# Kernel optimization log

Measured on AMD Instinct MI355X. Metric: run time of the kernel, lower is better.

## Reference

```python
import jax, jax.numpy as jnp
import numpy as np

N, D, H, F = 384, 512, 8, 64  # n_nodes, in/out features, heads, per-head hidden
SLOPE = 0.2


def gat_v2_layer(x, mask, W_l, W_r, a):
    """GATv2 layer (is_concat=True). x: [N, D_in]; mask: [N, N, 1] bool.

    torch semantics: g_sum[i, j] = g_l[j] + g_r[i]; e = a . LeakyReLU(g_sum);
    softmax over j (dim=1); aggregate g_r with einsum('ijh,jhf->ihf').
    attn linear nn.Linear(F, 1) is shared across heads -> a: [F].
    """
    n = x.shape[0]
    g_l = (x @ W_l).reshape(n, H, F)
    g_r = (x @ W_r).reshape(n, H, F)
    # pairwise [i, j, h, f] = g_r[i] + g_l[j]  (the big O(N^2) intermediate)
    s = jax.nn.leaky_relu(g_r[:, None] + g_l[None, :], negative_slope=SLOPE)
    e = jnp.einsum('ijhf,f->ijh', s, a)
    e = jnp.where(mask, e, -jnp.inf)
    att = jax.nn.softmax(e, axis=1)  # normalize over source nodes j
    out = jnp.einsum('ijh,jhf->ihf', att, g_r)
    return out.reshape(n, H * F)


def setup_inputs() -> dict:
    key = jax.random.key(0)
    ks = jax.random.split(key, 8)
    x = jax.random.normal(ks[0], (N, D), dtype=jnp.float32)
    adj = jax.random.randint(ks[1], (N, N, 1), 0, 2, dtype=jnp.int32)
    sd = 1.0 / np.sqrt(D)
    sa = 1.0 / np.sqrt(F)
    W_l0 = jax.random.normal(ks[2], (D, H * F), dtype=jnp.float32) * sd
    W_r0 = jax.random.normal(ks[3], (D, H * F), dtype=jnp.float32) * sd
    a0 = jax.random.normal(ks[4], (F,), dtype=jnp.float32) * sa
    W_l1 = jax.random.normal(ks[5], (H * F, H * F), dtype=jnp.float32) * sd
    W_r1 = jax.random.normal(ks[6], (H * F, H * F), dtype=jnp.float32) * sd
    a1 = jax.random.normal(ks[7], (F,), dtype=jnp.float32) * sa
    return {"x": x, "adj": adj, "W_l0": W_l0, "W_r0": W_r0, "a0": a0,
            "W_l1": W_l1, "W_r1": W_r1, "a1": a1}


def reference(x, adj, W_l0, W_r0, a0, W_l1, W_r1, a1):
    n = x.shape[0]
    # selfloop: fill diagonal of adj with 1
    idx = jnp.arange(n)
    adj = adj.at[idx, idx, 0].set(1)
    mask = adj != 0  # [N, N, 1]
    # layer 0: GATv2 -> ELU (i < n_layers-1) -> residual
    out = jax.nn.elu(gat_v2_layer(x, mask, W_l0, W_r0, a0))
    x = x + out
    # layer 1: GATv2 -> Identity -> residual
    out = gat_v2_layer(x, mask, W_l1, W_r1, a1)
    x = x + out
    return x
```

## Files before the change

kernel.cpp:

```cpp
#include <hip/hip_runtime.h>
#include <hip/hip_bf16.h>
#include <stdint.h>

typedef unsigned short ushort_t;
typedef unsigned long long u64;
typedef __attribute__((ext_vector_type(8))) short short8;
typedef __attribute__((ext_vector_type(4))) float f32x4;

#define N_NODES 384
#define HF      512
#define IT      12

__device__ inline ushort_t f2bf(float f) {
  __hip_bfloat16 b = __float2bfloat16(f);
  return *reinterpret_cast<ushort_t*>(&b);
}
__device__ inline float bf2f_u(ushort_t u) {
  union { float f; uint32_t i; } v; v.i = ((uint32_t)u) << 16; return v.f;
}
__device__ inline short8 pack8(const float* s) {
  short8 r;
#pragma unroll
  for (int j = 0; j < 8; ++j) r[j] = (short)f2bf(s[j]);
  return r;
}

__global__ __launch_bounds__(256) void gemm_direct(
    const float* __restrict__ X, const float* __restrict__ WL,
    const float* __restrict__ WR, float* __restrict__ G,
    ushort_t* __restrict__ glb, ushort_t* __restrict__ grT,
    const int* __restrict__ adj, u64* __restrict__ mbits)
{
  const int t = threadIdx.x, wave = t >> 6, lane = t & 63;
  const int lm = lane & 15, q = lane >> 4;
  const int m0 = blockIdx.x * 16;
  const int n0 = (blockIdx.y * 4 + wave) * 32;
  const float* Wp = (n0 < 512) ? (WL + n0) : (WR + (n0 - 512));
  const float* Arow = X + (m0 + lm) * HF;

  f32x4 acc0 = {0.f, 0.f, 0.f, 0.f};
  f32x4 acc1 = {0.f, 0.f, 0.f, 0.f};
#pragma unroll 4
  for (int kc = 0; kc < 16; ++kc) {
    const int kbase = kc * 32 + q * 8;
    float4 a0 = *(const float4*)(Arow + kbase);
    float4 a1 = *(const float4*)(Arow + kbase + 4);
    float av8[8] = {a0.x, a0.y, a0.z, a0.w, a1.x, a1.y, a1.z, a1.w};
    short8 af = pack8(av8);
    float b0f[8], b1f[8];
#pragma unroll
    for (int j = 0; j < 8; ++j) {
      const float* r = Wp + (kbase + j) * HF;
      b0f[j] = r[lm];
      b1f[j] = r[16 + lm];
    }
    short8 b0 = pack8(b0f);
    short8 b1 = pack8(b1f);
    acc0 = __builtin_amdgcn_mfma_f32_16x16x32_bf16(af, b0, acc0, 0, 0, 0);
    acc1 = __builtin_amdgcn_mfma_f32_16x16x32_bf16(af, b1, acc1, 0, 0, 0);
  }
  if (n0 < 512) {
#pragma unroll
    for (int r = 0; r < 4; ++r) {
      int m = m0 + q * 4 + r;
      glb[m * HF + n0 + lm]      = f2bf(acc0[r]);
      glb[m * HF + n0 + 16 + lm] = f2bf(acc1[r]);
    }
  } else {
#pragma unroll
    for (int r = 0; r < 4; ++r) {
      int m = m0 + q * 4 + r;
      G[m * 1024 + n0 + lm]      = acc0[r];
      G[m * 1024 + n0 + 16 + lm] = acc1[r];
    }
    int c0 = n0 - 512;
    uint2 p0, p1;
    p0.x = (uint32_t)f2bf(acc0[0]) | ((uint32_t)f2bf(acc0[1]) << 16);
    p0.y = (uint32_t)f2bf(acc0[2]) | ((uint32_t)f2bf(acc0[3]) << 16);
    p1.x = (uint32_t)f2bf(acc1[0]) | ((uint32_t)f2bf(acc1[1]) << 16);
    p1.y = (uint32_t)f2bf(acc1[2]) | ((uint32_t)f2bf(acc1[3]) << 16);
    *(uint2*)&grT[(c0 + lm) * 384 + m0 + q * 4]      = p0;
    *(uint2*)&grT[(c0 + 16 + lm) * 384 + m0 + q * 4] = p1;
  }
  if (adj != nullptr && blockIdx.y == 0) {
    int rbase = (blockIdx.x * 4 + wave) * 4;
    for (int rr = 0; rr < 4; ++rr) {
      int row = rbase + rr;
#pragma unroll
      for (int w = 0; w < 6; ++w) {
        int j = w * 64 + lane;
        u64 m = __ballot(adj[row * N_NODES + j] != 0 || row == j);
        if (lane == 0) mbits[row * 6 + w] = m;
      }
    }
  }
}

template <int LAYER>
__global__ __launch_bounds__(384) void attn_fused(
    const float* __restrict__ G, const ushort_t* __restrict__ glb,
    const ushort_t* __restrict__ grT, const u64* __restrict__ mbits,
    const float* __restrict__ resid_in, const float* __restrict__ avec,
    float* __restrict__ xcur_out, float* __restrict__ f_out)
{
  __shared__ __align__(16) char smem[55296];
  ushort_t (*s_gl)[72]     = (ushort_t(*)[72])smem;
  float    (*s_e)[N_NODES] = (float(*)[N_NODES])smem;
  ushort_t (*s_pb)[392]    = (ushort_t(*)[392])(smem + 18432);
  __shared__ float s_bri[IT];
  __shared__ u64   s_mask[IT][6];

  const int t = threadIdx.x;
  const int i0 = blockIdx.x * IT, h = blockIdx.y;
  const int lane = t & 63, wave = t >> 6;

  if (t < 72) ((u64*)s_mask)[t] = mbits[i0 * 6 + t];
  if (t >= 128 && t < 320) {
    int u = t - 128, il = u >> 4, fg = u & 15;
    float4 g4 = *(const float4*)(G + (i0 + il) * 1024 + 512 + h * 64 + fg * 4);
    float4 a4 = *(const float4*)(avec + fg * 4);
    float s = a4.x * g4.x + a4.y * g4.y + a4.z * g4.z + a4.w * g4.w;
    s += __shfl_xor(s, 1); s += __shfl_xor(s, 2);
    s += __shfl_xor(s, 4); s += __shfl_xor(s, 8);
    if (fg == 0) s_bri[il] = s;
  }
#pragma unroll
  for (int rep = 0; rep < 8; ++rep) {
    int idx = rep * 384 + t, row = idx >> 3, c = idx & 7;
    *(short8*)&s_gl[row][c * 8] =
        *(const short8*)&glb[row * HF + h * 64 + c * 8];
  }
  __syncthreads();

  float gl[64], av[64];
  {
    const short8* rowp = (const short8*)&s_gl[t][0];
#pragma unroll
    for (int c = 0; c < 8; ++c) {
      short8 v = rowp[c];
#pragma unroll
      for (int u2 = 0; u2 < 8; ++u2)
        gl[c * 8 + u2] = bf2f_u((ushort_t)v[u2]);
    }
#pragma unroll
    for (int c = 0; c < 16; ++c) {
      float4 a4 = ((const float4*)avec)[c];
      av[c * 4] = a4.x; av[c * 4 + 1] = a4.y;
      av[c * 4 + 2] = a4.z; av[c * 4 + 3] = a4.w;
    }
  }
  float accl = 0.f;
#pragma unroll
  for (int f = 0; f < 64; ++f) accl += av[f] * gl[f];
  __syncthreads();

  const int jw = t >> 6, jb = t & 63;
#pragma unroll
  for (int il = 0; il < IT; ++il) {
    const float4* gr4 = (const float4*)(G + (i0 + il) * 1024 + 512 + h * 64);
    float acc = 0.f;
#pragma unroll
    for (int c = 0; c < 16; ++c) {
      float4 g4 = gr4[c];
      acc += av[c * 4]     * fabsf(gl[c * 4]     + g4.x);
      acc += av[c * 4 + 1] * fabsf(gl[c * 4 + 1] + g4.y);
      acc += av[c * 4 + 2] * fabsf(gl[c * 4 + 2] + g4.z);
      acc += av[c * 4 + 3] * fabsf(gl[c * 4 + 3] + g4.w);
    }
    bool m = (s_mask[il][jw] >> jb) & 1;
    float e = 0.6f * (accl + s_bri[il]) + 0.4f * acc;
    s_e[il][t] = m ? e : -1e30f;
  }
#pragma unroll
  for (int r4 = 0; r4 < 4; ++r4) s_pb[IT + r4][t] = 0;
  __syncthreads();

  for (int il = wave; il < IT; il += 6) {
    float v[6];
    float mx = -1e30f;
#pragma unroll
    for (int c = 0; c < 6; ++c) { v[c] = s_e[il][lane + 64 * c]; mx = fmaxf(mx, v[c]); }
#pragma unroll
    for (int off = 32; off; off >>= 1) mx = fmaxf(mx, __shfl_xor(mx, off));
    float sum = 0.f;
#pragma unroll
    for (int c = 0; c < 6; ++c) { v[c] = __expf(v[c] - mx); sum += v[c]; }
#pragma unroll
    for (int off = 32; off; off >>= 1) sum += __shfl_xor(sum, off);
    float inv = 1.0f / sum;
#pragma unroll
    for (int c = 0; c < 6; ++c) s_pb[il][lane + 64 * c] = f2bf(v[c] * inv);
  }
  __syncthreads();

  if (wave < 4) {
    const int lm = lane & 15, q = lane >> 4;
    const int f0 = wave * 16;
    const ushort_t* Brow = grT + (h * 64 + f0 + lm) * 384;
    f32x4 acc = {0.f, 0.f, 0.f, 0.f};
#pragma unroll
    for (int kc = 0; kc < 12; ++kc) {
      short8 af = *(const short8*)&s_pb[lm][kc * 32 + q * 8];
      short8 bf = *(const short8*)&Brow[kc * 32 + q * 8];
      acc = __builtin_amdgcn_mfma_f32_16x16x32_bf16(af, bf, acc, 0, 0, 0);
    }
    if (q < 3) {
#pragma unroll
      for (int r = 0; r < 4; ++r) {
        int i = i0 + q * 4 + r;
        int off = i * HF + h * 64 + f0 + lm;
        float o = acc[r];
        if (LAYER == 0) {
          float oe = (o > 0.f) ? o : (__expf(o) - 1.f);
          xcur_out[off] = resid_in[off] + oe;
        } else {
          f_out[off] = resid_in[off] + o;
        }
      }
    }
  }
}

extern "C" void kernel_launch(void* const* d_in, const int* in_sizes, int n_in,
                              void* d_out, int out_size, void* d_ws, size_t ws_size,
                              hipStream_t stream) {
  const float* x   = (const float*)d_in[0];
  const int*   adj = (const int*)d_in[1];
  const float* Wl0 = (const float*)d_in[2];
  const float* Wr0 = (const float*)d_in[3];
  const float* a0  = (const float*)d_in[4];
  const float* Wl1 = (const float*)d_in[5];
  const float* Wr1 = (const float*)d_in[6];
  const float* a1  = (const float*)d_in[7];
  float* out = (float*)d_out;

  char* ws = (char*)d_ws;
  float*    G    = (float*)   (ws + 0L);
  ushort_t* grT  = (ushort_t*)(ws + (2L << 20));
  ushort_t* glb  = (ushort_t*)(ws + (3L << 20));
  u64*      mbits= (u64*)     (ws + (4L << 20));
  float*    xcur = (float*)   (ws + (5L << 20));

  gemm_direct<<<dim3(24, 8), 256, 0, stream>>>(x, Wl0, Wr0, G, glb, grT,
                                               adj, mbits);
  attn_fused<0><<<dim3(32, 8), 384, 0, stream>>>(G, glb, grT, mbits, x, a0,
                                                 xcur, nullptr);
  gemm_direct<<<dim3(24, 8), 256, 0, stream>>>(xcur, Wl1, Wr1, G, glb, grT,
                                               nullptr, nullptr);
  attn_fused<1><<<dim3(32, 8), 384, 0, stream>>>(G, glb, grT, mbits, xcur, a1,
                                                 nullptr, out);
}
```

Measured before the change: 124.1 us.

## Halve per-block work in GEMM and attention kernels to double grid size

The GEMM now has each wave compute a single 16x16 output tile instead of two, and the grid doubles in y to compensate. The attention kernel processes 6 target rows per block instead of 12, giving a 64x8 grid with one softmax row per wave. The s_pb buffer is moved, zero-padding is extended to fill the MFMA 16-row tile, and the attention vector is now read directly from global memory instead of register arrays. The aim is more blocks to fill the GPU's compute units and lower register pressure. The cost is more redundant loads of glb and W per block and extra launch overhead.

New measurement: 158.6 us. 1.28x slower.

```diff
diff --git a/kernel.cpp b/kernel.cpp
--- a/kernel.cpp
+++ b/kernel.cpp
@@ -9,7 +9,7 @@
 
 #define N_NODES 384
 #define HF      512
-#define IT      12
+#define IT      6
 
 __device__ inline ushort_t f2bf(float f) {
   __hip_bfloat16 b = __float2bfloat16(f);
@@ -34,12 +34,11 @@
   const int t = threadIdx.x, wave = t >> 6, lane = t & 63;
   const int lm = lane & 15, q = lane >> 4;
   const int m0 = blockIdx.x * 16;
-  const int n0 = (blockIdx.y * 4 + wave) * 32;
+  const int n0 = (blockIdx.y * 4 + wave) * 16;
   const float* Wp = (n0 < 512) ? (WL + n0) : (WR + (n0 - 512));
   const float* Arow = X + (m0 + lm) * HF;
 
-  f32x4 acc0 = {0.f, 0.f, 0.f, 0.f};
-  f32x4 acc1 = {0.f, 0.f, 0.f, 0.f};
+  f32x4 acc = {0.f, 0.f, 0.f, 0.f};
 #pragma unroll 4
   for (int kc = 0; kc < 16; ++kc) {
     const int kbase = kc * 32 + q * 8;
@@ -47,40 +46,25 @@
     float4 a1 = *(const float4*)(Arow + kbase + 4);
     float av8[8] = {a0.x, a0.y, a0.z, a0.w, a1.x, a1.y, a1.z, a1.w};
     short8 af = pack8(av8);
-    float b0f[8], b1f[8];
-#pragma unroll
-    for (int j = 0; j < 8; ++j) {
-      const float* r = Wp + (kbase + j) * HF;
-      b0f[j] = r[lm];
-      b1f[j] = r[16 + lm];
-    }
-    short8 b0 = pack8(b0f);
-    short8 b1 = pack8(b1f);
-    acc0 = __builtin_amdgcn_mfma_f32_16x16x32_bf16(af, b0, acc0, 0, 0, 0);
-    acc1 = __builtin_amdgcn_mfma_f32_16x16x32_bf16(af, b1, acc1, 0, 0, 0);
+    float bf8[8];
+#pragma unroll
+    for (int j = 0; j < 8; ++j) bf8[j] = Wp[(kbase + j) * HF + lm];
+    short8 b = pack8(bf8);
+    acc = __builtin_amdgcn_mfma_f32_16x16x32_bf16(af, b, acc, 0, 0, 0);
   }
   if (n0 < 512) {
 #pragma unroll
-    for (int r = 0; r < 4; ++r) {
-      int m = m0 + q * 4 + r;
-      glb[m * HF + n0 + lm]      = f2bf(acc0[r]);
-      glb[m * HF + n0 + 16 + lm] = f2bf(acc1[r]);
-    }
+    for (int r = 0; r < 4; ++r)
+      glb[(m0 + q * 4 + r) * HF + n0 + lm] = f2bf(acc[r]);
   } else {
 #pragma unroll
-    for (int r = 0; r < 4; ++r) {
-      int m = m0 + q * 4 + r;
-      G[m * 1024 + n0 + lm]      = acc0[r];
-      G[m * 1024 + n0 + 16 + lm] = acc1[r];
-    }
+    for (int r = 0; r < 4; ++r)
+      G[(m0 + q * 4 + r) * 1024 + n0 + lm] = acc[r];
     int c0 = n0 - 512;
-    uint2 p0, p1;
-    p0.x = (uint32_t)f2bf(acc0[0]) | ((uint32_t)f2bf(acc0[1]) << 16);
-    p0.y = (uint32_t)f2bf(acc0[2]) | ((uint32_t)f2bf(acc0[3]) << 16);
-    p1.x = (uint32_t)f2bf(acc1[0]) | ((uint32_t)f2bf(acc1[1]) << 16);
-    p1.y = (uint32_t)f2bf(acc1[2]) | ((uint32_t)f2bf(acc1[3]) << 16);
-    *(uint2*)&grT[(c0 + lm) * 384 + m0 + q * 4]      = p0;
-    *(uint2*)&grT[(c0 + 16 + lm) * 384 + m0 + q * 4] = p1;
+    uint2 p0;
+    p0.x = (uint32_t)f2bf(acc[0]) | ((uint32_t)f2bf(acc[1]) << 16);
+    p0.y = (uint32_t)f2bf(acc[2]) | ((uint32_t)f2bf(acc[3]) << 16);
+    *(uint2*)&grT[(c0 + lm) * 384 + m0 + q * 4] = p0;
   }
   if (adj != nullptr && blockIdx.y == 0) {
     int rbase = (blockIdx.x * 4 + wave) * 4;
@@ -106,7 +90,7 @@
   __shared__ __align__(16) char smem[55296];
   ushort_t (*s_gl)[72]     = (ushort_t(*)[72])smem;
   float    (*s_e)[N_NODES] = (float(*)[N_NODES])smem;
-  ushort_t (*s_pb)[392]    = (ushort_t(*)[392])(smem + 18432);
+  ushort_t (*s_pb)[392]    = (ushort_t(*)[392])(smem + 9216);
   __shared__ float s_bri[IT];
   __shared__ u64   s_mask[IT][6];
 
@@ -114,8 +98,8 @@
   const int i0 = blockIdx.x * IT, h = blockIdx.y;
   const int lane = t & 63, wave = t >> 6;
 
-  if (t < 72) ((u64*)s_mask)[t] = mbits[i0 * 6 + t];
-  if (t >= 128 && t < 320) {
+  if (t < 36) ((u64*)s_mask)[t] = mbits[i0 * 6 + t];
+  if (t >= 128 && t < 224) {
     int u = t - 128, il = u >> 4, fg = u & 15;
     float4 g4 = *(const float4*)(G + (i0 + il) * 1024 + 512 + h * 64 + fg * 4);
     float4 a4 = *(const float4*)(avec + fg * 4);
@@ -132,7 +116,7 @@
   }
   __syncthreads();
 
-  float gl[64], av[64];
+  float gl[64];
   {
     const short8* rowp = (const short8*)&s_gl[t][0];
 #pragma unroll
@@ -142,40 +126,30 @@
       for (int u2 = 0; u2 < 8; ++u2)
         gl[c * 8 + u2] = bf2f_u((ushort_t)v[u2]);
     }
-#pragma unroll
-    for (int c = 0; c < 16; ++c) {
-      float4 a4 = ((const float4*)avec)[c];
-      av[c * 4] = a4.x; av[c * 4 + 1] = a4.y;
-      av[c * 4 + 2] = a4.z; av[c * 4 + 3] = a4.w;
-    }
   }
   float accl = 0.f;
 #pragma unroll
-  for (int f = 0; f < 64; ++f) accl += av[f] * gl[f];
+  for (int f = 0; f < 64; ++f) accl += avec[f] * gl[f];
   __syncthreads();
 
   const int jw = t >> 6, jb = t & 63;
 #pragma unroll
   for (int il = 0; il < IT; ++il) {
-    const float4* gr4 = (const float4*)(G + (i0 + il) * 1024 + 512 + h * 64);
+    const float* __restrict__ grp = G + (i0 + il) * 1024 + 512 + h * 64;
     float acc = 0.f;
 #pragma unroll
-    for (int c = 0; c < 16; ++c) {
-      float4 g4 = gr4[c];
-      acc += av[c * 4]     * fabsf(gl[c * 4]     + g4.x);
-      acc += av[c * 4 + 1] * fabsf(gl[c * 4 + 1] + g4.y);
-      acc += av[c * 4 + 2] * fabsf(gl[c * 4 + 2] + g4.z);
-      acc += av[c * 4 + 3] * fabsf(gl[c * 4 + 3] + g4.w);
-    }
+    for (int f = 0; f < 64; ++f)
+      acc += avec[f] * fabsf(gl[f] + grp[f]);
     bool m = (s_mask[il][jw] >> jb) & 1;
     float e = 0.6f * (accl + s_bri[il]) + 0.4f * acc;
     s_e[il][t] = m ? e : -1e30f;
   }
 #pragma unroll
-  for (int r4 = 0; r4 < 4; ++r4) s_pb[IT + r4][t] = 0;
-  __syncthreads();
-
-  for (int il = wave; il < IT; il += 6) {
+  for (int r10 = 0; r10 < 10; ++r10) s_pb[IT + r10][t] = 0;
+  __syncthreads();
+
+  {
+    int il = wave;
     float v[6];
     float mx = -1e30f;
 #pragma unroll
@@ -204,9 +178,9 @@
       short8 bf = *(const short8*)&Brow[kc * 32 + q * 8];
       acc = __builtin_amdgcn_mfma_f32_16x16x32_bf16(af, bf, acc, 0, 0, 0);
     }
-    if (q < 3) {
-#pragma unroll
-      for (int r = 0; r < 4; ++r) {
+#pragma unroll
+    for (int r = 0; r < 4; ++r) {
+      if (q * 4 + r < IT) {
         int i = i0 + q * 4 + r;
         int off = i * HF + h * 64 + f0 + lm;
         float o = acc[r];
@@ -241,12 +215,12 @@
   u64*      mbits= (u64*)     (ws + (4L << 20));
   float*    xcur = (float*)   (ws + (5L << 20));
 
-  gemm_direct<<<dim3(24, 8), 256, 0, stream>>>(x, Wl0, Wr0, G, glb, grT,
-                                               adj, mbits);
-  attn_fused<0><<<dim3(32, 8), 384, 0, stream>>>(G, glb, grT, mbits, x, a0,
+  gemm_direct<<<dim3(24, 16), 256, 0, stream>>>(x, Wl0, Wr0, G, glb, grT,
+                                                adj, mbits);
+  attn_fused<0><<<dim3(64, 8), 384, 0, stream>>>(G, glb, grT, mbits, x, a0,
                                                  xcur, nullptr);
-  gemm_direct<<<dim3(24, 8), 256, 0, stream>>>(xcur, Wl1, Wr1, G, glb, grT,
-                                               nullptr, nullptr);
-  attn_fused<1><<<dim3(32, 8), 384, 0, stream>>>(G, glb, grT, mbits, xcur, a1,
+  gemm_direct<<<dim3(24, 16), 256, 0, stream>>>(xcur, Wl1, Wr1, G, glb, grT,
+                                                nullptr, nullptr);
+  attn_fused<1><<<dim3(64, 8), 384, 0, stream>>>(G, glb, grT, mbits, xcur, a1,
                                                  nullptr, out);
 }
```
